# Kernel tuning notes

Measured on AMD Instinct MI355X. Metric: run time of the kernel, lower is better.

## Reference

```python
import jax, jax.numpy as jnp
import numpy as np


def setup_inputs() -> dict:
    key = jax.random.key(0)
    k1, k2, k3, k4 = jax.random.split(key, 4)
    B, D, H, A, T = 1024, 512, 512, 18, 64
    xs = jax.random.normal(k1, (B, D), dtype=jnp.float32)
    task_id = jax.random.randint(k2, (B,), 0, T, dtype=jnp.int64)
    # weight_init ~ scaled randn; biases start at zero per the module
    fc1_weights = jax.random.normal(k3, (T, D, H), dtype=jnp.float32) * (1.0 / np.sqrt(D))
    fc1_biases = jnp.zeros((T, H), dtype=jnp.float32)
    fc2_weights = jax.random.normal(k4, (T, H, A), dtype=jnp.float32) * (1.0 / np.sqrt(H))
    fc2_biases = jnp.zeros((T, A), dtype=jnp.float32)
    return {"xs": xs, "task_id": task_id, "fc1_weights": fc1_weights,
            "fc1_biases": fc1_biases, "fc2_weights": fc2_weights, "fc2_biases": fc2_biases}


def reference(xs, task_id, fc1_weights, fc1_biases, fc2_weights, fc2_biases):
    # per-sample task-indexed weight gather (as in the torch module)
    w1 = fc1_weights[task_id]            # [B, D, H]
    b1 = fc1_biases[task_id]             # [B, H]
    w2 = fc2_weights[task_id]            # [B, H, A]
    b2 = fc2_biases[task_id]             # [B, A]
    h = jax.nn.relu(jnp.einsum('bd,bdh->bh', xs, w1) + b1)   # batch_linear + relu
    logits = jnp.einsum('bh,bha->ba', h, w2) + b2             # batch_linear
    logp = jax.nn.log_softmax(logits, axis=-1)                # [B, A]
    # Categorical sample (fixed key for reproducibility)
    action = jax.random.categorical(jax.random.key(1), logits, axis=-1)  # [B]
    log_prob = jnp.take_along_axis(logp, action[:, None], axis=1)        # [B, 1]
    entropy = -jnp.sum(jnp.exp(logp) * logp, axis=1, keepdims=True)      # [B, 1]
    return action, log_prob, entropy
```

## Files before the change

### kernel.cpp

```cpp
#include <hip/hip_runtime.h>
#include <stdint.h>

#define B_N   1024
#define D_DIM 512
#define H_DIM 512
#define A_DIM 18
#define T_N   64
#define HTILE 256
#define SMAX  32
#define NSB2  8

#define META_OFF   0
#define META_SLIST 256
#define META_INTS  2048

__device__ __forceinline__ bool taskid_is_int32(const int* raw, int lane) {
    int probe = raw[lane];
    unsigned long long odd = __ballot((lane & 1) && probe != 0);
    return odd != 0ull;
}

__global__ __launch_bounds__(1024) void bucket_kernel(const int* __restrict__ raw,
                                                      int* __restrict__ meta) {
    __shared__ int cnt[T_N];
    __shared__ int base[T_N];
    __shared__ int flag32;
    int tid = threadIdx.x;
    if (tid < 64) {
        bool is32 = taskid_is_int32(raw, tid);
        if (tid == 0) flag32 = is32 ? 1 : 0;
    }
    if (tid < T_N) cnt[tid] = 0;
    __syncthreads();
    int id = flag32 ? raw[tid] : raw[2 * tid];
    atomicAdd(&cnt[id], 1);
    __syncthreads();
    if (tid < 64) {
        int v = cnt[tid];
        int x = v;
#pragma unroll
        for (int o = 1; o < 64; o <<= 1) {
            int tv = __shfl_up(x, o);
            if (tid >= o) x += tv;
        }
        int excl = x - v;
        meta[META_OFF + tid] = excl;
        base[tid] = excl;
        if (tid == 63) meta[META_OFF + 64] = x;
    }
    __syncthreads();
    int pos = atomicAdd(&base[id], 1);
    meta[META_SLIST + pos] = tid;
}

template <int KSP>
__global__ __launch_bounds__(256) void fc1_kernel(const float* __restrict__ xs,
                                                  const float* __restrict__ w1,
                                                  const int* __restrict__ meta,
                                                  float* __restrict__ hpre) {
    constexpr int DK = D_DIM / KSP;
    constexpr int NCHUNK = DK / 8;
    int task  = blockIdx.x;
    int htile = blockIdx.y;
    int ksp   = blockIdx.z;
    int tid   = threadIdx.x;
    int lane  = tid & 63;
    int wv4   = tid >> 6;

    int off0 = meta[META_OFF + task];
    int n    = meta[META_OFF + task + 1] - off0;
    if (n == 0) return;

    const int* slist = meta + META_SLIST + off0;

    __shared__ __align__(16) float xlds[SMAX][DK];
    __shared__ __align__(16) float wlds[2][8][HTILE];

    int hbase = htile * HTILE + lane * 4;
    int d0    = ksp * DK;
    const float* wtile = w1 + ((size_t)task * D_DIM + d0) * H_DIM + htile * HTILE;
    float* hout = hpre + (size_t)ksp * ((size_t)B_N * H_DIM);

    int r0row = tid >> 6;
    int r0col = (tid & 63) * 4;
    int r1row = 4 + (tid >> 6);
    int r1col = r0col;

#define WLOAD(cc, rrow, rcol) \
    (*(const float4*)(wtile + (size_t)((cc) * 8 + (rrow)) * H_DIM + (rcol)))

    for (int sbase = 0; sbase < n; sbase += SMAX) {
        int ns = min(SMAX, n - sbase);

        for (int idx = tid; idx < SMAX * (DK / 4); idx += 256) {
            int sl = idx / (DK / 4);
            int f  = idx - sl * (DK / 4);
            if (sl < ns) {
                int smp = slist[sbase + sl];
                *(float4*)(&xlds[sl][4 * f]) =
                    *(const float4*)(xs + (size_t)smp * D_DIM + d0 + 4 * f);
            }
        }

        float4 acc[SMAX / 4];
#pragma unroll
        for (int j = 0; j < SMAX / 4; ++j) acc[j] = make_float4(0.f, 0.f, 0.f, 0.f);

        float4 s0 = WLOAD(0, r0row, r0col);
        float4 s1 = WLOAD(0, r1row, r1col);
        __syncthreads();

        int buf = 0;
        for (int c = 0; c < NCHUNK; ++c) {
            *(float4*)(&wlds[buf][r0row][r0col]) = s0;
            *(float4*)(&wlds[buf][r1row][r1col]) = s1;
            if (c + 1 < NCHUNK) {
                s0 = WLOAD(c + 1, r0row, r0col);
                s1 = WLOAD(c + 1, r1row, r1col);
            }
            __syncthreads();

            float4 wvr[8];
#pragma unroll
            for (int u = 0; u < 8; ++u)
                wvr[u] = *(const float4*)(&wlds[buf][u][lane * 4]);
            int d = c * 8;
#pragma unroll
            for (int j = 0; j < SMAX / 4; ++j) {
                int sl = wv4 + 4 * j;
                if (sl < ns) {
                    const float* xp = &xlds[sl][d];
                    float4 xa = *(const float4*)xp;
                    float4 xb = *(const float4*)(xp + 4);
                    float xv[8] = {xa.x, xa.y, xa.z, xa.w, xb.x, xb.y, xb.z, xb.w};
#pragma unroll
                    for (int u = 0; u < 8; ++u) {
                        acc[j].x = fmaf(xv[u], wvr[u].x, acc[j].x);
                        acc[j].y = fmaf(xv[u], wvr[u].y, acc[j].y);
                        acc[j].z = fmaf(xv[u], wvr[u].z, acc[j].z);
                        acc[j].w = fmaf(xv[u], wvr[u].w, acc[j].w);
                    }
                }
            }
            buf ^= 1;
        }
#undef WLOAD

#pragma unroll
        for (int j = 0; j < SMAX / 4; ++j) {
            int sl = wv4 + 4 * j;
            if (sl < ns) {
                int smp = slist[sbase + sl];
                *(float4*)(hout + (size_t)smp * H_DIM + hbase) = acc[j];
            }
        }
        __syncthreads();
    }
}

__device__ __forceinline__ uint32_t rotl32(uint32_t x, int r) {
    return (x << r) | (x >> (32 - r));
}

__device__ __forceinline__ uint32_t threefry_bits_part(uint32_t i) {
    uint32_t x0 = 0u;
    uint32_t x1 = i;
    const uint32_t ks0 = 0u, ks1 = 1u, ks2 = 0x1BD11BDAu ^ 0u ^ 1u;
    x0 += ks0; x1 += ks1;
#define TFR(r) { x0 += x1; x1 = rotl32(x1, (r)); x1 ^= x0; }
    TFR(13) TFR(15) TFR(26) TFR(6)
    x0 += ks1; x1 += ks2 + 1u;
    TFR(17) TFR(29) TFR(16) TFR(24)
    x0 += ks2; x1 += ks0 + 2u;
    TFR(13) TFR(15) TFR(26) TFR(6)
    x0 += ks0; x1 += ks1 + 3u;
    TFR(17) TFR(29) TFR(16) TFR(24)
    x0 += ks1; x1 += ks2 + 4u;
    TFR(13) TFR(15) TFR(26) TFR(6)
    x0 += ks2; x1 += ks0 + 5u;
#undef TFR
    return x0 ^ x1;
}

template <int KSP>
__global__ __launch_bounds__(256) void head_kernel(const int* __restrict__ meta,
                                                   const float* __restrict__ hpre,
                                                   const float* __restrict__ b1,
                                                   const float* __restrict__ w2,
                                                   const float* __restrict__ b2,
                                                   float* __restrict__ out) {
    __shared__ __align__(16) float w2l[H_DIM * A_DIM];
    __shared__ float red[4][16][A_DIM];
    __shared__ float logits_lds[4][A_DIM];

    int t    = blockIdx.x;
    int y    = blockIdx.y;
    int tid  = threadIdx.x;
    int lane = tid & 63;
    int wv   = tid >> 6;

    int off0 = meta[META_OFF + t];
    int n    = meta[META_OFF + t + 1] - off0;
    if (4 * y >= n) return;
    int K = (n - 4 * y - 1) / 32 + 1;

    const int* slist = meta + META_SLIST + off0;

    const float4* g4 = (const float4*)(w2 + (size_t)t * (H_DIM * A_DIM));
    float4* l4 = (float4*)w2l;
#pragma unroll
    for (int i = 0; i < (H_DIM * A_DIM) / (256 * 4); ++i)
        l4[i * 256 + tid] = g4[i * 256 + tid];
    __syncthreads();

    for (int rnd = 0; rnd < K; ++rnd) {
        int slot = 4 * y + wv + 32 * rnd;
        bool active = slot < n;
        int s = active ? slist[slot] : 0;

        float hreg[H_DIM / 64];
#pragma unroll
        for (int kk = 0; kk < H_DIM / 64; ++kk) {
            int h = lane + 64 * kk;
            size_t p = (size_t)s * H_DIM + h;
            float v = b1[(size_t)t * H_DIM + h];
#pragma unroll
            for (int q = 0; q < KSP; ++q)
                v += hpre[(size_t)q * ((size_t)B_N * H_DIM) + p];
            hreg[kk] = fmaxf(v, 0.f);
        }

        float la[A_DIM];
#pragma unroll
        for (int a = 0; a < A_DIM; ++a) la[a] = 0.f;
#pragma unroll
        for (int kk = 0; kk < H_DIM / 64; ++kk) {
            int h = lane + 64 * kk;
            const float2* row = (const float2*)&w2l[h * A_DIM];
            float hk = hreg[kk];
#pragma unroll
            for (int a2 = 0; a2 < A_DIM / 2; ++a2) {
                float2 ww = row[a2];
                la[2 * a2]     = fmaf(hk, ww.x, la[2 * a2]);
                la[2 * a2 + 1] = fmaf(hk, ww.y, la[2 * a2 + 1]);
            }
        }

#pragma unroll
        for (int a = 0; a < A_DIM; ++a) {
            la[a] += __shfl_xor(la[a], 1);
            la[a] += __shfl_xor(la[a], 2);
        }
        if ((lane & 3) == 0) {
            int g = lane >> 2;
#pragma unroll
            for (int a = 0; a < A_DIM; ++a) red[wv][g][a] = la[a];
        }
        __syncthreads();
        if (lane < A_DIM) {
            float sum = b2[(size_t)t * A_DIM + lane];
#pragma unroll
            for (int g = 0; g < 16; ++g) sum += red[wv][g][lane];
            logits_lds[wv][lane] = sum;
        }
        __syncthreads();

        float lg = (lane < A_DIM) ? logits_lds[wv][lane] : -INFINITY;

        float z = -INFINITY;
        if (lane < A_DIM) {
            uint32_t bits = threefry_bits_part((uint32_t)(s * A_DIM + lane));
            float f = __uint_as_float(0x3f800000u | (bits >> 9)) - 1.0f;
            float u = fmaxf(f, 1.17549435e-38f);
            float g = -logf(-logf(u));
            z = lg + g;
        }
        int idx = lane;
#pragma unroll
        for (int o = 1; o < 64; o <<= 1) {
            float oz = __shfl_xor(z, o);
            int   oi = __shfl_xor(idx, o);
            if (oz > z || (oz == z && oi < idx)) { z = oz; idx = oi; }
        }

        float mx = lg;
#pragma unroll
        for (int o = 1; o < 64; o <<= 1) mx = fmaxf(mx, __shfl_xor(mx, o));
        float e = (lane < A_DIM) ? expf(lg - mx) : 0.f;
#pragma unroll
        for (int o = 1; o < 64; o <<= 1) e += __shfl_xor(e, o);
        float lse = mx + logf(e);
        float lp = lg - lse;
        float c = (lane < A_DIM) ? expf(lp) * lp : 0.f;
#pragma unroll
        for (int o = 1; o < 64; o <<= 1) c += __shfl_xor(c, o);

        if (active && lane == 0) {
            out[s]             = (float)idx;
            out[B_N + s]       = logits_lds[wv][idx] - lse;
            out[2 * B_N + s]   = -c;
        }
        __syncthreads();
    }
}

extern "C" void kernel_launch(void* const* d_in, const int* in_sizes, int n_in,
                              void* d_out, int out_size, void* d_ws, size_t ws_size,
                              hipStream_t stream) {
    const float* xs      = (const float*)d_in[0];
    const int*   traw    = (const int*)d_in[1];
    const float* w1      = (const float*)d_in[2];
    const float* b1      = (const float*)d_in[3];
    const float* w2      = (const float*)d_in[4];
    const float* b2      = (const float*)d_in[5];
    float* out = (float*)d_out;
    char*  ws  = (char*)d_ws;

    const size_t meta_bytes = META_INTS * sizeof(int);
    const size_t part_bytes = (size_t)B_N * H_DIM * sizeof(float);

    int ksp = 4;
    if (ws_size < meta_bytes + 4 * part_bytes) ksp = 2;
    if (ws_size < meta_bytes + 2 * part_bytes) ksp = 1;

    int*   meta = (int*)ws;
    float* hpre = (float*)(ws + meta_bytes);

    bucket_kernel<<<1, 1024, 0, stream>>>(traw, meta);

    if (ksp == 4) {
        fc1_kernel<4><<<dim3(T_N, 2, 4), 256, 0, stream>>>(xs, w1, meta, hpre);
        head_kernel<4><<<dim3(T_N, NSB2), 256, 0, stream>>>(meta, hpre, b1, w2, b2, out);
    } else if (ksp == 2) {
        fc1_kernel<2><<<dim3(T_N, 2, 2), 256, 0, stream>>>(xs, w1, meta, hpre);
        head_kernel<2><<<dim3(T_N, NSB2), 256, 0, stream>>>(meta, hpre, b1, w2, b2, out);
    } else {
        fc1_kernel<1><<<dim3(T_N, 2, 1), 256, 0, stream>>>(xs, w1, meta, hpre);
        head_kernel<1><<<dim3(T_N, NSB2), 256, 0, stream>>>(meta, hpre, b1, w2, b2, out);
    }
}
```

Measured before the change: 125.4 us.

## Drop bucket kernel; rebuild per-task sample list in each block via ballots

The separate single-block bucketing kernel is removed. Each fc1 and head block now scans all 1024 task ids itself, using wave ballots and popcounts to build its task's sample list in shared memory. This removes one kernel launch and the serial dependency on it, at the cost of every block redundantly reading the task id array. The head grid is also halved from 8 to 4 y-blocks per task, and the final barrier in fc1 is skipped on the last iteration.

```diff
diff --git a/kernel.cpp b/kernel.cpp
--- a/kernel.cpp
+++ b/kernel.cpp
@@ -8,11 +8,6 @@
 #define T_N   64
 #define HTILE 256
 #define SMAX  32
-#define NSB2  8
-
-#define META_OFF   0
-#define META_SLIST 256
-#define META_INTS  2048
 
 __device__ __forceinline__ bool taskid_is_int32(const int* raw, int lane) {
     int probe = raw[lane];
@@ -20,43 +15,45 @@
     return odd != 0ull;
 }
 
-__global__ __launch_bounds__(1024) void bucket_kernel(const int* __restrict__ raw,
-                                                      int* __restrict__ meta) {
-    __shared__ int cnt[T_N];
-    __shared__ int base[T_N];
-    __shared__ int flag32;
-    int tid = threadIdx.x;
-    if (tid < 64) {
-        bool is32 = taskid_is_int32(raw, tid);
-        if (tid == 0) flag32 = is32 ? 1 : 0;
-    }
-    if (tid < T_N) cnt[tid] = 0;
+__device__ __forceinline__ int build_slist(const int* __restrict__ raw, int task,
+                                           int* slist, int* wcnt,
+                                           int tid) {
+    int lane = tid & 63;
+    int wv   = tid >> 6;
+    bool is32 = taskid_is_int32(raw, lane);
+
+    int cnt = 0;
+#pragma unroll
+    for (int c = 0; c < 4; ++c) {
+        int i  = 256 * wv + 64 * c + lane;
+        int id = is32 ? raw[i] : raw[2 * i];
+        cnt += __popcll(__ballot(id == task));
+    }
+    if (lane == 0) wcnt[wv] = cnt;
     __syncthreads();
-    int id = flag32 ? raw[tid] : raw[2 * tid];
-    atomicAdd(&cnt[id], 1);
+    int n = wcnt[0] + wcnt[1] + wcnt[2] + wcnt[3];
+    int base = 0;
+    for (int w = 0; w < wv; ++w) base += wcnt[w];
+
+#pragma unroll
+    for (int c = 0; c < 4; ++c) {
+        int i  = 256 * wv + 64 * c + lane;
+        int id = is32 ? raw[i] : raw[2 * i];
+        unsigned long long m = __ballot(id == task);
+        if (id == task) {
+            unsigned long long below = m & ((1ull << lane) - 1ull);
+            slist[base + __popcll(below)] = i;
+        }
+        base += __popcll(m);
+    }
     __syncthreads();
-    if (tid < 64) {
-        int v = cnt[tid];
-        int x = v;
-#pragma unroll
-        for (int o = 1; o < 64; o <<= 1) {
-            int tv = __shfl_up(x, o);
-            if (tid >= o) x += tv;
-        }
-        int excl = x - v;
-        meta[META_OFF + tid] = excl;
-        base[tid] = excl;
-        if (tid == 63) meta[META_OFF + 64] = x;
-    }
-    __syncthreads();
-    int pos = atomicAdd(&base[id], 1);
-    meta[META_SLIST + pos] = tid;
+    return n;
 }
 
 template <int KSP>
 __global__ __launch_bounds__(256) void fc1_kernel(const float* __restrict__ xs,
                                                   const float* __restrict__ w1,
-                                                  const int* __restrict__ meta,
+                                                  const int* __restrict__ raw,
                                                   float* __restrict__ hpre) {
     constexpr int DK = D_DIM / KSP;
     constexpr int NCHUNK = DK / 8;
@@ -67,14 +64,13 @@
     int lane  = tid & 63;
     int wv4   = tid >> 6;
 
-    int off0 = meta[META_OFF + task];
-    int n    = meta[META_OFF + task + 1] - off0;
-    if (n == 0) return;
-
-    const int* slist = meta + META_SLIST + off0;
-
+    __shared__ int slist[B_N];
+    __shared__ int wcnt[4];
     __shared__ __align__(16) float xlds[SMAX][DK];
     __shared__ __align__(16) float wlds[2][8][HTILE];
+
+    int n = build_slist(raw, task, slist, wcnt, tid);
+    if (n == 0) return;
 
     int hbase = htile * HTILE + lane * 4;
     int d0    = ksp * DK;
@@ -154,7 +150,7 @@
                 *(float4*)(hout + (size_t)smp * H_DIM + hbase) = acc[j];
             }
         }
-        __syncthreads();
+        if (sbase + SMAX < n) __syncthreads();
     }
 }
 
@@ -183,12 +179,14 @@
 }
 
 template <int KSP>
-__global__ __launch_bounds__(256) void head_kernel(const int* __restrict__ meta,
+__global__ __launch_bounds__(256) void head_kernel(const int* __restrict__ raw,
                                                    const float* __restrict__ hpre,
                                                    const float* __restrict__ b1,
                                                    const float* __restrict__ w2,
                                                    const float* __restrict__ b2,
                                                    float* __restrict__ out) {
+    __shared__ int slist[B_N];
+    __shared__ int wcnt[4];
     __shared__ __align__(16) float w2l[H_DIM * A_DIM];
     __shared__ float red[4][16][A_DIM];
     __shared__ float logits_lds[4][A_DIM];
@@ -199,12 +197,9 @@
     int lane = tid & 63;
     int wv   = tid >> 6;
 
-    int off0 = meta[META_OFF + t];
-    int n    = meta[META_OFF + t + 1] - off0;
+    int n = build_slist(raw, t, slist, wcnt, tid);
     if (4 * y >= n) return;
-    int K = (n - 4 * y - 1) / 32 + 1;
-
-    const int* slist = meta + META_SLIST + off0;
+    int K = (n - 4 * y - 1) / 16 + 1;
 
     const float4* g4 = (const float4*)(w2 + (size_t)t * (H_DIM * A_DIM));
     float4* l4 = (float4*)w2l;
@@ -214,7 +209,7 @@
     __syncthreads();
 
     for (int rnd = 0; rnd < K; ++rnd) {
-        int slot = 4 * y + wv + 32 * rnd;
+        int slot = 4 * y + wv + 16 * rnd;
         bool active = slot < n;
         int s = active ? slist[slot] : 0;
 
@@ -316,26 +311,22 @@
     float* out = (float*)d_out;
     char*  ws  = (char*)d_ws;
 
-    const size_t meta_bytes = META_INTS * sizeof(int);
     const size_t part_bytes = (size_t)B_N * H_DIM * sizeof(float);
 
     int ksp = 4;
-    if (ws_size < meta_bytes + 4 * part_bytes) ksp = 2;
-    if (ws_size < meta_bytes + 2 * part_bytes) ksp = 1;
-
-    int*   meta = (int*)ws;
-    float* hpre = (float*)(ws + meta_bytes);
-
-    bucket_kernel<<<1, 1024, 0, stream>>>(traw, meta);
+    if (ws_size < 4 * part_bytes) ksp = 2;
+    if (ws_size < 2 * part_bytes) ksp = 1;
+
+    float* hpre = (float*)ws;
 
     if (ksp == 4) {
-        fc1_kernel<4><<<dim3(T_N, 2, 4), 256, 0, stream>>>(xs, w1, meta, hpre);
-        head_kernel<4><<<dim3(T_N, NSB2), 256, 0, stream>>>(meta, hpre, b1, w2, b2, out);
+        fc1_kernel<4><<<dim3(T_N, 2, 4), 256, 0, stream>>>(xs, w1, traw, hpre);
+        head_kernel<4><<<dim3(T_N, 4), 256, 0, stream>>>(traw, hpre, b1, w2, b2, out);
     } else if (ksp == 2) {
-        fc1_kernel<2><<<dim3(T_N, 2, 2), 256, 0, stream>>>(xs, w1, meta, hpre);
-        head_kernel<2><<<dim3(T_N, NSB2), 256, 0, stream>>>(meta, hpre, b1, w2, b2, out);
+        fc1_kernel<2><<<dim3(T_N, 2, 2), 256, 0, stream>>>(xs, w1, traw, hpre);
+        head_kernel<2><<<dim3(T_N, 4), 256, 0, stream>>>(traw, hpre, b1, w2, b2, out);
     } else {
-        fc1_kernel<1><<<dim3(T_N, 2, 1), 256, 0, stream>>>(xs, w1, meta, hpre);
-        head_kernel<1><<<dim3(T_N, NSB2), 256, 0, stream>>>(meta, hpre, b1, w2, b2, out);
-    }
-}
+        fc1_kernel<1><<<dim3(T_N, 2, 1), 256, 0, stream>>>(xs, w1, traw, hpre);
+        head_kernel<1><<<dim3(T_N, 4), 256, 0, stream>>>(traw, hpre, b1, w2, b2, out);
+    }
+}
```

New measurement: 124.0 us. No clear change (-1.1%).
